# Optimization experiments

Measured on AMD Instinct MI355X. Metric: run time of the kernel, lower is better.

## Reference

```python
import jax, jax.numpy as jnp
import numpy as np

N_NODES = 50000
N_EDGES = 800000
NODE_DIM = 128
EDGE_DIM = 64
HIDDEN = 256


def setup_inputs() -> dict:
    key = jax.random.key(0)
    ks = jax.random.split(key, 12)
    glorot = lambda k, fi, fo: jax.random.normal(k, (fi, fo), jnp.float32) * (2.0 / (fi + fo)) ** 0.5
    return {
        "node_features": jax.random.normal(ks[0], (N_NODES, NODE_DIM), jnp.float32),
        "edge_features": jax.random.normal(ks[1], (N_EDGES, EDGE_DIM), jnp.float32),
        "src": jax.random.randint(ks[2], (N_EDGES,), 0, N_NODES),
        "dst": jax.random.randint(ks[3], (N_EDGES,), 0, N_NODES),
        # edge_update MLP: (2*node_dim + edge_dim) -> hidden -> edge_dim
        "We1": glorot(ks[4], 2 * NODE_DIM + EDGE_DIM, HIDDEN),
        "be1": jnp.zeros((HIDDEN,), jnp.float32),
        "We2": glorot(ks[5], HIDDEN, EDGE_DIM),
        "be2": jnp.zeros((EDGE_DIM,), jnp.float32),
        # node_update MLP: (node_dim + edge_dim) -> hidden -> node_dim
        "Wn1": glorot(ks[6], NODE_DIM + EDGE_DIM, HIDDEN),
        "bn1": jnp.zeros((HIDDEN,), jnp.float32),
        "Wn2": glorot(ks[7], HIDDEN, NODE_DIM),
        "bn2": jnp.zeros((NODE_DIM,), jnp.float32),
    }


def reference(node_features, edge_features, src, dst, We1, be1, We2, be2, Wn1, bn1, Wn2, bn2):
    # message: per-edge MLP on [src_h, e, dst_h]
    concat = jnp.concatenate(
        [node_features[src], edge_features, node_features[dst]], axis=1
    )  # [E, 2*node_dim + edge_dim]
    e_upd = jax.nn.relu(concat @ We1 + be1) @ We2 + be2  # [E, edge_dim]

    # reduce: sum incoming messages per destination node
    e_sum = jax.ops.segment_sum(e_upd, dst, num_segments=node_features.shape[0])  # [N, edge_dim]
    node_in = jnp.concatenate([node_features, e_sum], axis=1)  # [N, node_dim + edge_dim]
    h_new = jax.nn.relu(node_in @ Wn1 + bn1) @ Wn2 + bn2  # [N, node_dim]

    # DGL only applies reduce_func to nodes with at least one incoming edge
    deg = jax.ops.segment_sum(jnp.ones_like(dst, jnp.float32), dst, num_segments=node_features.shape[0])
    h_out = jnp.where(deg[:, None] > 0, h_new, node_features)

    # original module never writes e_updated back: returned edge features are the inputs
    return h_out, edge_features
```

## Files before the change

### kernel.cpp

```cpp
#include <hip/hip_runtime.h>

#define N_NODES 50000
#define N_EDGES 800000
#define NODE_DIM 128
#define EDGE_DIM 64
#define HIDDEN 256
#define K_E 320
#define K_N 192

typedef __attribute__((ext_vector_type(8))) short bf16x8;
typedef __attribute__((ext_vector_type(4))) float f32x4;
typedef __attribute__((ext_vector_type(16))) float f32x16;
typedef unsigned short u16;
typedef unsigned int u32;

#define MFMA16 __builtin_amdgcn_mfma_f32_16x16x32_bf16
#define MFMA32 __builtin_amdgcn_mfma_f32_32x32x16_bf16

__device__ inline u16 f2bf(float f) {
  u32 u = __builtin_bit_cast(u32, f);
  u += 0x7fffu + ((u >> 16) & 1u);
  return (u16)(u >> 16);
}
__device__ inline float bf2f(u16 u) {
  u32 x = ((u32)u) << 16;
  return __builtin_bit_cast(float, x);
}
__device__ inline u32 pack2(float a, float b) {
  return (u32)f2bf(a) | ((u32)f2bf(b) << 16);
}
__device__ inline void st_bf4(u16* p, float4 v) {
  ushort4 r;
  r.x = f2bf(v.x); r.y = f2bf(v.y); r.z = f2bf(v.z); r.w = f2bf(v.w);
  *reinterpret_cast<ushort4*>(p) = r;
}

__global__ void prep_weights(const float* __restrict__ We1, const float* __restrict__ We2,
                             const float* __restrict__ Wn1, const float* __restrict__ Wn2,
                             const float* __restrict__ nf, const int* __restrict__ dst,
                             u16* __restrict__ w1y, u16* __restrict__ w2y,
                             u16* __restrict__ wn1t, u16* __restrict__ wn2t,
                             u16* __restrict__ nfb, int* __restrict__ hist) {
  const int stride = gridDim.x * blockDim.x;
  const int tid = blockIdx.x * blockDim.x + threadIdx.x;
  for (int i = tid; i < HIDDEN * K_E; i += stride) {
    int jj = i & 7;
    int l = (i >> 3) & 63;
    int rem = i % 10240;
    int kb = rem >> 9;
    int ht = i / 10240;
    int h = ht * 32 + (l & 31);
    int k = kb * 16 + (l >> 5) * 8 + jj;
    w1y[i] = f2bf(We1[k * HIDDEN + h]);
  }
  for (int i = tid; i < EDGE_DIM * HIDDEN; i += stride) {
    int jj = i & 7;
    int l = (i >> 3) & 63;
    int t2 = (i >> 9) & 1;
    int kb2 = i >> 10;
    int out = t2 * 32 + (l & 31);
    int hi = l >> 5;
    int k = kb2 * 16 + (jj & 3) + 8 * (jj >> 2) + 4 * hi;
    w2y[i] = f2bf(We2[k * EDGE_DIM + out]);
  }
  for (int i = tid; i < HIDDEN * K_N; i += stride) {
    int n = i / K_N, k = i % K_N;
    wn1t[i] = f2bf(Wn1[k * HIDDEN + n]);
  }
  for (int i = tid; i < NODE_DIM * HIDDEN; i += stride) {
    int n = i / HIDDEN, k = i % HIDDEN;
    wn2t[i] = f2bf(Wn2[k * NODE_DIM + n]);
  }
  {
    const float4* nf4 = reinterpret_cast<const float4*>(nf);
    for (int i = tid; i < N_NODES * NODE_DIM / 4; i += stride)
      st_bf4(&nfb[i * 4], nf4[i]);
  }
  for (int i = tid; i < N_EDGES; i += stride)
    atomicAdd(&hist[dst[i]], 1);
}

#define NB_SCAN 196

__global__ void scanA_kernel(const int* __restrict__ hist, int* __restrict__ eid) {
  __shared__ int red[256];
  int gid = blockIdx.x * 256 + threadIdx.x;
  int v = (gid < N_NODES) ? hist[gid] : 0;
  red[threadIdx.x] = v;
  __syncthreads();
  for (int d = 128; d > 0; d >>= 1) {
    if (threadIdx.x < d) red[threadIdx.x] += red[threadIdx.x + d];
    __syncthreads();
  }
  if (threadIdx.x == 0) eid[blockIdx.x] = red[0];
}

__global__ void scanB_kernel(int* __restrict__ eid, int* __restrict__ off) {
  __shared__ int ssum[256];
  int tid = threadIdx.x;
  int v = (tid < NB_SCAN) ? eid[tid] : 0;
  ssum[tid] = v;
  __syncthreads();
  for (int d = 1; d < 256; d <<= 1) {
    int t = (tid >= d) ? ssum[tid - d] : 0;
    __syncthreads();
    ssum[tid] += t;
    __syncthreads();
  }
  if (tid < NB_SCAN) eid[256 + tid] = ssum[tid] - v;
  if (tid == 255) off[N_NODES] = ssum[255];
}

__global__ void scanC_kernel(const int* __restrict__ hist, const int* __restrict__ eid,
                             int* __restrict__ off, int* __restrict__ cursor) {
  __shared__ int ssum[256];
  int tid = threadIdx.x;
  int gid = blockIdx.x * 256 + tid;
  int base = eid[256 + blockIdx.x];
  int v = (gid < N_NODES) ? hist[gid] : 0;
  ssum[tid] = v;
  __syncthreads();
  for (int d = 1; d < 256; d <<= 1) {
    int t = (tid >= d) ? ssum[tid - d] : 0;
    __syncthreads();
    ssum[tid] += t;
    __syncthreads();
  }
  if (gid < N_NODES) {
    int o = base + ssum[tid] - v;
    off[gid] = o;
    cursor[gid] = o;
  }
}

__global__ void scatter_kernel(const int* __restrict__ src, const int* __restrict__ dst,
                               int* __restrict__ cursor, int* __restrict__ eid,
                               int* __restrict__ csr_src, int* __restrict__ csr_dst) {
  int e = blockIdx.x * blockDim.x + threadIdx.x;
  if (e < N_EDGES) {
    int d = dst[e];
    int pos = atomicAdd(&cursor[d], 1);
    eid[pos] = e;
    csr_src[pos] = src[e];
    csr_dst[pos] = d;
  }
}

__global__ __launch_bounds__(256, 3) void edge_mlp(
    const u16* __restrict__ nfb, const float* __restrict__ ef,
    const int* __restrict__ eid, const int* __restrict__ csr_src,
    const int* __restrict__ csr_dst,
    const u16* __restrict__ w1y, const float* __restrict__ b1,
    const u16* __restrict__ w2y, const float* __restrict__ b2,
    float* __restrict__ e_sum, float* __restrict__ out_edge)
{
  __shared__ u16 W1s[2][10240];

  const int tid = threadIdx.x;
  const int wv = tid >> 6, lane = tid & 63;
  const int ecol = lane & 31;
  const int hi = lane >> 5;
  const int e0 = blockIdx.x * 128;
  const int pos = e0 + wv * 32 + ecol;

  {
    const float4* ef4 = reinterpret_cast<const float4*>(ef);
    float4* oe4 = reinterpret_cast<float4*>(out_edge);
    #pragma unroll
    for (int p = 0; p < 8; ++p) {
      size_t i = (size_t)e0 * 16 + p * 256 + tid;
      oe4[i] = ef4[i];
    }
  }

  const int e    = eid[pos];
  const int srcn = csr_src[pos];
  const int dstn = csr_dst[pos];

  const int si = srcn << 7;
  const int di = dstn << 7;
  bf16x8 efr[20];
  #pragma unroll
  for (int kb = 0; kb < 8; ++kb)
    efr[kb] = *reinterpret_cast<const bf16x8*>(nfb + si + kb * 16 + hi * 8);
  #pragma unroll
  for (int kb = 0; kb < 4; ++kb) {
    const float* ep = ef + (size_t)e * 64 + kb * 16 + hi * 8;
    float4 lo = *reinterpret_cast<const float4*>(ep);
    float4 hv = *reinterpret_cast<const float4*>(ep + 4);
    bf16x8 v;
    v[0] = (short)f2bf(lo.x); v[1] = (short)f2bf(lo.y);
    v[2] = (short)f2bf(lo.z); v[3] = (short)f2bf(lo.w);
    v[4] = (short)f2bf(hv.x); v[5] = (short)f2bf(hv.y);
    v[6] = (short)f2bf(hv.z); v[7] = (short)f2bf(hv.w);
    efr[8 + kb] = v;
  }
  #pragma unroll
  for (int kb = 0; kb < 8; ++kb)
    efr[12 + kb] = *reinterpret_cast<const bf16x8*>(nfb + di + kb * 16 + hi * 8);

  {
    const uint4* s = reinterpret_cast<const uint4*>(w1y);
    uint4* d = reinterpret_cast<uint4*>(W1s[0]);
    #pragma unroll
    for (int j = 0; j < 5; ++j) d[tid + j * 256] = s[tid + j * 256];
  }
  __syncthreads();

  f32x16 acc2[2];
  #pragma unroll
  for (int t2 = 0; t2 < 2; ++t2)
    #pragma unroll
    for (int r = 0; r < 16; ++r)
      acc2[t2][r] = b2[t2 * 32 + (r & 3) + 8 * (r >> 2) + 4 * hi];

  #pragma unroll
  for (int ht = 0; ht < 8; ++ht) {
    uint4 st[5];
    if (ht < 7) {
      const uint4* s = reinterpret_cast<const uint4*>(w1y + (ht + 1) * 10240);
      #pragma unroll
      for (int j = 0; j < 5; ++j) st[j] = s[tid + j * 256];
    }

    f32x16 acc;
    #pragma unroll
    for (int r = 0; r < 16; ++r)
      acc[r] = b1[ht * 32 + (r & 3) + 8 * (r >> 2) + 4 * hi];
    const u16* Wb = W1s[ht & 1];
    #pragma unroll
    for (int kb = 0; kb < 20; ++kb) {
      bf16x8 wf = *reinterpret_cast<const bf16x8*>(Wb + (kb * 64 + lane) * 8);
      acc = MFMA32(wf, efr[kb], acc, 0, 0, 0);
    }

    #pragma unroll
    for (int s2 = 0; s2 < 2; ++s2) {
      bf16x8 hf;
      u32* hw = reinterpret_cast<u32*>(&hf);
      #pragma unroll
      for (int m = 0; m < 4; ++m)
        hw[m] = pack2(fmaxf(acc[s2 * 8 + 2 * m], 0.f),
                      fmaxf(acc[s2 * 8 + 2 * m + 1], 0.f));
      #pragma unroll
      for (int t2 = 0; t2 < 2; ++t2) {
        bf16x8 wf2 = *reinterpret_cast<const bf16x8*>(
            w2y + ((size_t)((ht * 2 + s2) * 2 + t2) * 64 + lane) * 8);
        acc2[t2] = MFMA32(wf2, hf, acc2[t2], 0, 0, 0);
      }
    }

    if (ht < 7) {
      uint4* d = reinterpret_cast<uint4*>(W1s[(ht + 1) & 1]);
      #pragma unroll
      for (int j = 0; j < 5; ++j) d[tid + j * 256] = st[j];
      __syncthreads();
    }
  }

  __syncthreads();

  float* bounce = reinterpret_cast<float*>(W1s);
  {
    const int lp = wv * 32 + ecol;
    #pragma unroll
    for (int t2 = 0; t2 < 2; ++t2)
      #pragma unroll
      for (int r = 0; r < 16; ++r) {
        int o = t2 * 32 + (r & 3) + 8 * (r >> 2) + 4 * hi;
        bounce[lp * 65 + o] = acc2[t2][r];
      }
  }
  __syncthreads();

  {
    const int d = lane;
    const int base = wv * 32;
    float s = bounce[base * 65 + d];
    int cur = __shfl(dstn, 0, 64);
    #pragma unroll 4
    for (int i = 1; i < 32; ++i) {
      int nx = __shfl(dstn, i, 64);
      float v = bounce[(base + i) * 65 + d];
      if (nx == cur) {
        s += v;
      } else {
        atomicAdd(&e_sum[(size_t)cur * 64 + d], s);
        cur = nx;
        s = v;
      }
    }
    atomicAdd(&e_sum[(size_t)cur * 64 + d], s);
  }
}

#define SA_N 200
#define SH   264

__global__ __launch_bounds__(256) void node_kernel(
    const float* __restrict__ nf, const float* __restrict__ e_sum,
    const int* __restrict__ hist,
    const u16* __restrict__ w1, const float* __restrict__ b1,
    const u16* __restrict__ w2, const float* __restrict__ b2,
    float* __restrict__ hout)
{
  __shared__ u16 A[64 * SH];
  const int tid = threadIdx.x;
  const int n0 = blockIdx.x * 64;

  const float4* nf4 = reinterpret_cast<const float4*>(nf);
  const float4* es4 = reinterpret_cast<const float4*>(e_sum);

  #pragma unroll
  for (int p = 0; p < 8; ++p) {
    int i = p * 256 + tid;
    int row = i >> 5, c4 = i & 31;
    int rg = min(n0 + row, N_NODES - 1);
    float4 v = nf4[(size_t)rg * 32 + c4];
    st_bf4(&A[row * SA_N + c4 * 4], v);
  }
  #pragma unroll
  for (int p = 0; p < 4; ++p) {
    int i = p * 256 + tid;
    int row = i >> 4, c4 = i & 15;
    int rg = min(n0 + row, N_NODES - 1);
    float4 v = es4[(size_t)rg * 16 + c4];
    st_bf4(&A[row * SA_N + 128 + c4 * 4], v);
  }
  __syncthreads();

  const int wave = tid >> 6, lane = tid & 63;
  const int lr = lane & 15;
  const int lk = (lane >> 4) * 8;

  f32x4 acc[4][4] = {};
  for (int kb = 0; kb < K_N / 32; ++kb) {
    const int ko = kb * 32 + lk;
    bf16x8 a[4], b[4];
    #pragma unroll
    for (int mt = 0; mt < 4; ++mt)
      a[mt] = *reinterpret_cast<const bf16x8*>(&A[(mt * 16 + lr) * SA_N + ko]);
    #pragma unroll
    for (int nt = 0; nt < 4; ++nt)
      b[nt] = *reinterpret_cast<const bf16x8*>(&w1[(size_t)(wave * 64 + nt * 16 + lr) * K_N + ko]);
    #pragma unroll
    for (int mt = 0; mt < 4; ++mt)
      #pragma unroll
      for (int nt = 0; nt < 4; ++nt)
        acc[mt][nt] = MFMA16(a[mt], b[nt], acc[mt][nt], 0, 0, 0);
  }
  __syncthreads();

  u16* H = A;
  #pragma unroll
  for (int mt = 0; mt < 4; ++mt)
    #pragma unroll
    for (int nt = 0; nt < 4; ++nt) {
      int col = wave * 64 + nt * 16 + lr;
      float bias = b1[col];
      #pragma unroll
      for (int j = 0; j < 4; ++j) {
        int row = mt * 16 + (lane >> 4) * 4 + j;
        float h = acc[mt][nt][j] + bias;
        H[row * SH + col] = f2bf(h > 0.f ? h : 0.f);
      }
    }
  __syncthreads();

  f32x4 acc2[8] = {};
  for (int kb = 0; kb < HIDDEN / 32; ++kb) {
    const int ko = kb * 32 + lk;
    bf16x8 a = *reinterpret_cast<const bf16x8*>(&H[(wave * 16 + lr) * SH + ko]);
    #pragma unroll
    for (int nt = 0; nt < 8; ++nt) {
      bf16x8 b = *reinterpret_cast<const bf16x8*>(&w2[(size_t)(nt * 16 + lr) * HIDDEN + ko]);
      acc2[nt] = MFMA16(a, b, acc2[nt], 0, 0, 0);
    }
  }
  #pragma unroll
  for (int nt = 0; nt < 8; ++nt) {
    int col = nt * 16 + lr;
    float bias = b2[col];
    #pragma unroll
    for (int j = 0; j < 4; ++j) {
      int row = wave * 16 + (lane >> 4) * 4 + j;
      int rg = n0 + row;
      if (rg < N_NODES) {
        float v = acc2[nt][j] + bias;
        hout[(size_t)rg * NODE_DIM + col] =
            (hist[rg] != 0) ? v : nf[(size_t)rg * NODE_DIM + col];
      }
    }
  }
}

extern "C" void kernel_launch(void* const* d_in, const int* in_sizes, int n_in,
                              void* d_out, int out_size, void* d_ws, size_t ws_size,
                              hipStream_t stream) {
  const float* nf  = (const float*)d_in[0];
  const float* ef  = (const float*)d_in[1];
  const int*   src = (const int*)d_in[2];
  const int*   dst = (const int*)d_in[3];
  const float* We1 = (const float*)d_in[4];
  const float* be1 = (const float*)d_in[5];
  const float* We2 = (const float*)d_in[6];
  const float* be2 = (const float*)d_in[7];
  const float* Wn1 = (const float*)d_in[8];
  const float* bn1 = (const float*)d_in[9];
  const float* Wn2 = (const float*)d_in[10];
  const float* bn2 = (const float*)d_in[11];

  float* hout = (float*)d_out;
  float* out_edge = hout + (size_t)N_NODES * NODE_DIM;

  char* ws = (char*)d_ws;
  int*   hist    = (int*)ws;
  int*   off     = (int*)(ws + 200000);
  int*   cursor  = (int*)(ws + 400016);
  int*   eid     = (int*)(ws + 600016);
  int*   csr_src = (int*)(ws + 3800016);
  int*   csr_dst = (int*)(ws + 7000016);
  float* e_sum   = (float*)(ws + 10200016);
  u16*   w1y     = (u16*)(ws + 23000016);
  u16*   w2y     = (u16*)(ws + 23163856);
  u16*   wn1t    = (u16*)(ws + 23196624);
  u16*   wn2t    = (u16*)(ws + 23294928);
  u16*   nfb     = (u16*)(ws + 23360464);

  hipMemsetAsync(hist, 0, 200000, stream);
  hipMemsetAsync(e_sum, 0, 12800000, stream);
  prep_weights<<<512, 256, 0, stream>>>(We1, We2, Wn1, Wn2, nf, dst,
                                        w1y, w2y, wn1t, wn2t, nfb, hist);
  scanA_kernel<<<NB_SCAN, 256, 0, stream>>>(hist, eid);
  scanB_kernel<<<1, 256, 0, stream>>>(eid, off);
  scanC_kernel<<<NB_SCAN, 256, 0, stream>>>(hist, eid, off, cursor);
  scatter_kernel<<<(N_EDGES + 255) / 256, 256, 0, stream>>>(src, dst, cursor, eid,
                                                            csr_src, csr_dst);

  edge_mlp<<<N_EDGES / 128, 256, 0, stream>>>(nfb, ef, eid, csr_src, csr_dst,
                                              w1y, be1, w2y, be2, e_sum, out_edge);
  node_kernel<<<(N_NODES + 63) / 64, 256, 0, stream>>>(nf, e_sum, hist,
                                                       wn1t, bn1, wn2t, bn2, hout);
}
```

Before: 591.1 us.

## Read edge MLP weights directly from global memory instead of LDS double-buffering

Removes the double-buffered LDS staging of the first-layer edge weights, along with its per-tile __syncthreads barriers. Each wave now loads its MFMA weight fragments straight from global memory, relying on L1/L2 caching. Biases are pre-permuted in the prep kernel so each lane loads them contiguously. The epilogue uses a dedicated LDS bounce buffer with no block barrier, since each wave only touches its own rows. The risk is roughly four times more cache traffic for weights, because the four waves no longer share one LDS copy.

```diff
diff --git a/kernel.cpp b/kernel.cpp
--- a/kernel.cpp
+++ b/kernel.cpp
@@ -37,9 +37,11 @@
 
 __global__ void prep_weights(const float* __restrict__ We1, const float* __restrict__ We2,
                              const float* __restrict__ Wn1, const float* __restrict__ Wn2,
+                             const float* __restrict__ be1, const float* __restrict__ be2,
                              const float* __restrict__ nf, const int* __restrict__ dst,
                              u16* __restrict__ w1y, u16* __restrict__ w2y,
                              u16* __restrict__ wn1t, u16* __restrict__ wn2t,
+                             float* __restrict__ b1p, float* __restrict__ b2p,
                              u16* __restrict__ nfb, int* __restrict__ hist) {
   const int stride = gridDim.x * blockDim.x;
   const int tid = blockIdx.x * blockDim.x + threadIdx.x;
@@ -71,6 +73,14 @@
     int n = i / HIDDEN, k = i % HIDDEN;
     wn2t[i] = f2bf(Wn2[k * NODE_DIM + n]);
   }
+  for (int i = tid; i < HIDDEN; i += stride) {
+    int ht = i >> 5, hi = (i >> 4) & 1, r = i & 15;
+    b1p[i] = be1[ht * 32 + (r & 3) + 8 * (r >> 2) + 4 * hi];
+  }
+  for (int i = tid; i < EDGE_DIM; i += stride) {
+    int t2 = i >> 5, hi = (i >> 4) & 1, r = i & 15;
+    b2p[i] = be2[t2 * 32 + (r & 3) + 8 * (r >> 2) + 4 * hi];
+  }
   {
     const float4* nf4 = reinterpret_cast<const float4*>(nf);
     for (int i = tid; i < N_NODES * NODE_DIM / 4; i += stride)
@@ -150,11 +160,11 @@
     const u16* __restrict__ nfb, const float* __restrict__ ef,
     const int* __restrict__ eid, const int* __restrict__ csr_src,
     const int* __restrict__ csr_dst,
-    const u16* __restrict__ w1y, const float* __restrict__ b1,
-    const u16* __restrict__ w2y, const float* __restrict__ b2,
+    const u16* __restrict__ w1y, const float* __restrict__ b1p,
+    const u16* __restrict__ w2y, const float* __restrict__ b2p,
     float* __restrict__ e_sum, float* __restrict__ out_edge)
 {
-  __shared__ u16 W1s[2][10240];
+  __shared__ float bounce[128 * 65];
 
   const int tid = threadIdx.x;
   const int wv = tid >> 6, lane = tid & 63;
@@ -199,35 +209,23 @@
   for (int kb = 0; kb < 8; ++kb)
     efr[12 + kb] = *reinterpret_cast<const bf16x8*>(nfb + di + kb * 16 + hi * 8);
 
-  {
-    const uint4* s = reinterpret_cast<const uint4*>(w1y);
-    uint4* d = reinterpret_cast<uint4*>(W1s[0]);
-    #pragma unroll
-    for (int j = 0; j < 5; ++j) d[tid + j * 256] = s[tid + j * 256];
-  }
-  __syncthreads();
-
   f32x16 acc2[2];
   #pragma unroll
-  for (int t2 = 0; t2 < 2; ++t2)
-    #pragma unroll
-    for (int r = 0; r < 16; ++r)
-      acc2[t2][r] = b2[t2 * 32 + (r & 3) + 8 * (r >> 2) + 4 * hi];
+  for (int t2 = 0; t2 < 2; ++t2) {
+    const float* bp = b2p + t2 * 32 + hi * 16;
+    #pragma unroll
+    for (int r = 0; r < 16; ++r) acc2[t2][r] = bp[r];
+  }
 
   #pragma unroll
   for (int ht = 0; ht < 8; ++ht) {
-    uint4 st[5];
-    if (ht < 7) {
-      const uint4* s = reinterpret_cast<const uint4*>(w1y + (ht + 1) * 10240);
-      #pragma unroll
-      for (int j = 0; j < 5; ++j) st[j] = s[tid + j * 256];
-    }
-
     f32x16 acc;
-    #pragma unroll
-    for (int r = 0; r < 16; ++r)
-      acc[r] = b1[ht * 32 + (r & 3) + 8 * (r >> 2) + 4 * hi];
-    const u16* Wb = W1s[ht & 1];
+    {
+      const float* bp = b1p + ht * 32 + hi * 16;
+      #pragma unroll
+      for (int r = 0; r < 16; ++r) acc[r] = bp[r];
+    }
+    const u16* Wb = w1y + ht * 10240;
     #pragma unroll
     for (int kb = 0; kb < 20; ++kb) {
       bf16x8 wf = *reinterpret_cast<const bf16x8*>(Wb + (kb * 64 + lane) * 8);
@@ -249,18 +247,8 @@
         acc2[t2] = MFMA32(wf2, hf, acc2[t2], 0, 0, 0);
       }
     }
-
-    if (ht < 7) {
-      uint4* d = reinterpret_cast<uint4*>(W1s[(ht + 1) & 1]);
-      #pragma unroll
-      for (int j = 0; j < 5; ++j) d[tid + j * 256] = st[j];
-      __syncthreads();
-    }
-  }
-
-  __syncthreads();
-
-  float* bounce = reinterpret_cast<float*>(W1s);
+  }
+
   {
     const int lp = wv * 32 + ecol;
     #pragma unroll
@@ -271,7 +259,6 @@
         bounce[lp * 65 + o] = acc2[t2][r];
       }
   }
-  __syncthreads();
 
   {
     const int d = lane;
@@ -425,12 +412,14 @@
   u16*   w2y     = (u16*)(ws + 23163856);
   u16*   wn1t    = (u16*)(ws + 23196624);
   u16*   wn2t    = (u16*)(ws + 23294928);
-  u16*   nfb     = (u16*)(ws + 23360464);
+  float* b1p     = (float*)(ws + 23360464);
+  float* b2p     = (float*)(ws + 23361488);
+  u16*   nfb     = (u16*)(ws + 23361744);
 
   hipMemsetAsync(hist, 0, 200000, stream);
   hipMemsetAsync(e_sum, 0, 12800000, stream);
-  prep_weights<<<512, 256, 0, stream>>>(We1, We2, Wn1, Wn2, nf, dst,
-                                        w1y, w2y, wn1t, wn2t, nfb, hist);
+  prep_weights<<<512, 256, 0, stream>>>(We1, We2, Wn1, Wn2, be1, be2, nf, dst,
+                                        w1y, w2y, wn1t, wn2t, b1p, b2p, nfb, hist);
   scanA_kernel<<<NB_SCAN, 256, 0, stream>>>(hist, eid);
   scanB_kernel<<<1, 256, 0, stream>>>(eid, off);
   scanC_kernel<<<NB_SCAN, 256, 0, stream>>>(hist, eid, off, cursor);
@@ -438,7 +427,7 @@
                                                             csr_src, csr_dst);
 
   edge_mlp<<<N_EDGES / 128, 256, 0, stream>>>(nfb, ef, eid, csr_src, csr_dst,
-                                              w1y, be1, w2y, be2, e_sum, out_edge);
+                                              w1y, b1p, w2y, b2p, e_sum, out_edge);
   node_kernel<<<(N_NODES + 63) / 64, 256, 0, stream>>>(nf, e_sum, hist,
                                                        wn1t, bn1, wn2t, bn2, hout);
 }
```

Result: slower. 777.4 us (+31.5%).
